# Kernel tuning notes

Measured on AMD Instinct MI355X. Metric: run time of the kernel, lower is better.

## Reference

```python
import jax, jax.numpy as jnp
import numpy as np

D_MODEL = 1024
N_HEADS = 16
D_HEAD = D_MODEL // N_HEADS
D_FF = 4096
THETA = 10000.0
EPS = 1e-5


def rmsnorm(x, g):
    xf = x.astype(jnp.float32)
    rms = jnp.sqrt(jnp.mean(xf * xf, axis=-1, keepdims=True) + EPS)
    return ((xf / rms) * g).astype(x.dtype)


def rope(x, pos):
    # x: (B, H, S, d_head); pos: (S,) int
    dk = x.shape[-1]
    inv_freq = 1.0 / (THETA ** (jnp.arange(0, dk, 2, dtype=jnp.float32) / dk))
    freqs = pos.astype(jnp.float32)[:, None] * inv_freq[None, :]  # (S, dk/2)
    cos, sin = jnp.cos(freqs), jnp.sin(freqs)
    xp = x.reshape(*x.shape[:-1], dk // 2, 2)
    xe, xo = xp[..., 0], xp[..., 1]
    re = xe * cos - xo * sin
    ro = xe * sin + xo * cos
    return jnp.stack([re, ro], axis=-1).reshape(x.shape)


def attention(x, pos, q_w, k_w, v_w, o_w):
    B, S, D = x.shape
    def heads(t):
        return t.reshape(B, S, N_HEADS, D_HEAD).transpose(0, 2, 1, 3)
    Q = heads(x @ q_w.T)
    K = heads(x @ k_w.T)
    V = heads(x @ v_w.T)
    Q = rope(Q, pos)
    K = rope(K, pos)
    scores = jnp.einsum('bhqd,bhkd->bhqk', Q, K) / jnp.sqrt(jnp.float32(D_HEAD))
    causal = jnp.tril(jnp.ones((S, S), dtype=bool))
    scores = jnp.where(causal[None, None], scores, -jnp.inf)
    attn = jax.nn.softmax(scores, axis=-1)
    H = jnp.einsum('bhqk,bhkd->bhqd', attn, V)
    H = H.transpose(0, 2, 1, 3).reshape(B, S, D)
    return H @ o_w.T


def swiglu(x, w1, w2, w3):
    a = x @ w1.T
    swish = a * jax.nn.sigmoid(a)
    gate = x @ w3.T
    return (swish * gate) @ w2.T


def setup_inputs() -> dict:
    key = jax.random.key(0)
    ks = jax.random.split(key, 8)
    B, S = 4, 2048
    std_ff = (2.0 / (D_MODEL + D_FF)) ** 0.5
    return {
        'x': jax.random.normal(ks[0], (B, S, D_MODEL), jnp.float32),
        'token_positions': jnp.arange(S, dtype=jnp.int32),
        'q_w': jax.random.truncated_normal(ks[1], -3, 3, (D_MODEL, D_MODEL), jnp.float32),
        'k_w': jax.random.truncated_normal(ks[2], -3, 3, (D_MODEL, D_MODEL), jnp.float32),
        'v_w': jax.random.truncated_normal(ks[3], -3, 3, (D_MODEL, D_MODEL), jnp.float32),
        'o_w': jax.random.truncated_normal(ks[4], -3, 3, (D_MODEL, D_MODEL), jnp.float32),
        'g1': jnp.ones((D_MODEL,), jnp.float32),
        'g2': jnp.ones((D_MODEL,), jnp.float32),
        'w1': jax.random.truncated_normal(ks[5], -3, 3, (D_FF, D_MODEL), jnp.float32) * std_ff,
        'w2': jax.random.truncated_normal(ks[6], -3, 3, (D_MODEL, D_FF), jnp.float32) * std_ff,
        'w3': jax.random.truncated_normal(ks[7], -3, 3, (D_FF, D_MODEL), jnp.float32) * std_ff,
    }


def reference(x, token_positions, q_w, k_w, v_w, o_w, g1, g2, w1, w2, w3):
    x_norm = rmsnorm(x, g1)
    O = x + attention(x_norm, token_positions, q_w, k_w, v_w, o_w)
    H = O + swiglu(rmsnorm(O, g2), w1, w2, w3)
    return H
```

## Files before the change

kernel.cpp:

```cpp
#include <hip/hip_runtime.h>
#include <stdint.h>


typedef short bf16x8 __attribute__((ext_vector_type(8)));
typedef float f32x4  __attribute__((ext_vector_type(4)));

#define DEV static __device__ __forceinline__

DEV float bf2f(uint32_t u) { uint32_t v = u << 16; float f; __builtin_memcpy(&f, &v, 4); return f; }
DEV uint16_t f2bf(float f) {
  uint32_t u; __builtin_memcpy(&u, &f, 4);
  u = (u + 0x7fffu + ((u >> 16) & 1u)) >> 16;
  return (uint16_t)u;
}

DEV void gl_lds16(const uint16_t* g, uint16_t* l) {
  __builtin_amdgcn_global_load_lds((const __attribute__((address_space(1))) uint32_t*)g,
                                   (__attribute__((address_space(3))) uint32_t*)l, 16, 0, 0);
}


__global__ __launch_bounds__(256) void cvt_bf16_k(const float* __restrict__ src,
                                                  uint16_t* __restrict__ dst, int n4) {
  const int t = blockIdx.x * 256 + threadIdx.x;
  if (t >= n4) return;
  const float4 v = ((const float4*)src)[t];
  ushort4 o; o.x = f2bf(v.x); o.y = f2bf(v.y); o.z = f2bf(v.z); o.w = f2bf(v.w);
  ((ushort4*)dst)[t] = o;
}

__global__ __launch_bounds__(256) void cvt_split_qk_k(const float* __restrict__ qw,
                                                      const float* __restrict__ kw,
                                                      uint16_t* __restrict__ hi,
                                                      uint16_t* __restrict__ lo) {
  const int t = blockIdx.x * 256 + threadIdx.x;
  const int row = t >> 8, c4 = t & 255;
  const float* src = (row < 1024) ? (qw + (size_t)row * 1024)
                                  : (kw + (size_t)(row - 1024) * 1024);
  const float4 v = ((const float4*)src)[c4];
  ushort4 h, l;
  h.x = f2bf(v.x); l.x = f2bf(v.x - bf2f(h.x));
  h.y = f2bf(v.y); l.y = f2bf(v.y - bf2f(h.y));
  h.z = f2bf(v.z); l.z = f2bf(v.z - bf2f(h.z));
  h.w = f2bf(v.w); l.w = f2bf(v.w - bf2f(h.w));
  ((ushort4*)hi)[t] = h; ((ushort4*)lo)[t] = l;
}


__global__ __launch_bounds__(256) void cs_tab_k(const int* __restrict__ pos,
                                                float2* __restrict__ tab) {
  const int t = blockIdx.x * 256 + threadIdx.x;
  const int p = t >> 5, d2 = t & 31;
  const float inv_freq = exp2f((float)d2 * -0.41524101186092029f);
  float sn, cs; sincosf((float)pos[p] * inv_freq, &sn, &cs);
  tab[t] = make_float2(cs, sn);
}


template <bool SPLIT>
__global__ __launch_bounds__(256) void rmsnorm_k(const float* __restrict__ xin,
                                                 const float* __restrict__ g,
                                                 uint16_t* __restrict__ hi,
                                                 uint16_t* __restrict__ lo) {
  const int row = blockIdx.x, t = threadIdx.x;
  const float4 v = ((const float4*)(xin + (size_t)row * 1024))[t];
  float ss = v.x * v.x + v.y * v.y + v.z * v.z + v.w * v.w;
#pragma unroll
  for (int m = 1; m < 64; m <<= 1) ss += __shfl_xor(ss, m);
  __shared__ float red[4];
  if ((t & 63) == 0) red[t >> 6] = ss;
  __syncthreads();
  const float rinv = rsqrtf((red[0] + red[1] + red[2] + red[3]) * (1.0f / 1024.0f) + 1e-5f);
  const float4 gv = ((const float4*)g)[t];
  float y[4] = { v.x * rinv * gv.x, v.y * rinv * gv.y, v.z * rinv * gv.z, v.w * rinv * gv.w };
  ushort4 h; h.x = f2bf(y[0]); h.y = f2bf(y[1]); h.z = f2bf(y[2]); h.w = f2bf(y[3]);
  ((ushort4*)(hi + (size_t)row * 1024))[t] = h;
  if constexpr (SPLIT) {
    ushort4 l;
    l.x = f2bf(y[0] - bf2f(h.x)); l.y = f2bf(y[1] - bf2f(h.y));
    l.z = f2bf(y[2] - bf2f(h.z)); l.w = f2bf(y[3] - bf2f(h.w));
    ((ushort4*)(lo + (size_t)row * 1024))[t] = l;
  }
}


template <int OUT>
__global__ __launch_bounds__(256) void gemm_bt_k(const uint16_t* __restrict__ A,
                                                 const uint16_t* __restrict__ B,
                                                 void* __restrict__ C,
                                                 const float* __restrict__ resid,
                                                 int N, int K) {
  __shared__ __align__(16) uint16_t As[128 * 64];
  __shared__ __align__(16) uint16_t Bs[128 * 64];
  const int t = threadIdx.x, w = t >> 6, lane = t & 63, m16 = lane & 15, quad = lane >> 4;
  const int wm = (w >> 1) * 64, wn = (w & 1) * 64;
  const int mBase = blockIdx.y * 128, nBase = blockIdx.x * 128;
  f32x4 acc[4][4];
  const f32x4 vz = {0.f, 0.f, 0.f, 0.f};
#pragma unroll
  for (int i = 0; i < 4; ++i)
#pragma unroll
    for (int j = 0; j < 4; ++j) acc[i][j] = vz;
  const int r_ = t >> 3, g_ = t & 7, sg = g_ ^ (r_ & 7);
  const uint16_t* ag = A + (size_t)(mBase + r_) * K + sg * 8;
  const uint16_t* bg = B + (size_t)(nBase + r_) * K + sg * 8;
  for (int k0 = 0; k0 < K; k0 += 64) {
#pragma unroll
    for (int it = 0; it < 4; ++it) {
      gl_lds16(ag + (size_t)(it * 32) * K + k0, As + it * 2048 + t * 8);
      gl_lds16(bg + (size_t)(it * 32) * K + k0, Bs + it * 2048 + t * 8);
    }
    __syncthreads();
#pragma unroll
    for (int ks = 0; ks < 2; ++ks) {
      bf16x8 af[4], bf4[4];
      const int cg = ks * 4 + quad;
#pragma unroll
      for (int i = 0; i < 4; ++i) {
        const int rA = wm + i * 16 + m16;
        af[i] = *(const bf16x8*)(As + rA * 64 + ((cg ^ (rA & 7)) * 8));
        const int rB = wn + i * 16 + m16;
        bf4[i] = *(const bf16x8*)(Bs + rB * 64 + ((cg ^ (rB & 7)) * 8));
      }
#pragma unroll
      for (int i = 0; i < 4; ++i)
#pragma unroll
        for (int j = 0; j < 4; ++j)
          acc[i][j] = __builtin_amdgcn_mfma_f32_16x16x32_bf16(af[i], bf4[j], acc[i][j], 0, 0, 0);
    }
    __syncthreads();
  }
#pragma unroll
  for (int i = 0; i < 4; ++i) {
    const int row0 = mBase + wm + i * 16 + quad * 4;
#pragma unroll
    for (int j = 0; j < 4; ++j) {
      const int col = nBase + wn + j * 16 + m16;
#pragma unroll
      for (int r = 0; r < 4; ++r) {
        const size_t idx = (size_t)(row0 + r) * N + col;
        const float v = acc[i][j][r];
        if constexpr (OUT == 1) ((float*)C)[idx] = v + resid[idx];
        else                    ((uint16_t*)C)[idx] = f2bf(v);
      }
    }
  }
}


template <int OUT>
__global__ __launch_bounds__(512, 2) void gemm256_k(const uint16_t* __restrict__ A,
                                                    const uint16_t* __restrict__ B,
                                                    uint16_t* __restrict__ C,
                                                    const uint16_t* __restrict__ aux,
                                                    int N, int K) {
  __shared__ __align__(16) uint16_t As[2][256 * 64];
  __shared__ __align__(16) uint16_t Bs[2][256 * 64];
  const int t = threadIdx.x, w = t >> 6, lane = t & 63, m16 = lane & 15, quad = lane >> 4;
  const int wm = (w >> 2) * 128, wn = (w & 3) * 64;
  const int mBase = blockIdx.y * 256, nBase = blockIdx.x * 256;
  const int NT = K >> 6;

  f32x4 acc[8][4];
  const f32x4 vz = {0.f, 0.f, 0.f, 0.f};
#pragma unroll
  for (int i = 0; i < 8; ++i)
#pragma unroll
    for (int j = 0; j < 4; ++j) acc[i][j] = vz;

  const int r_ = t >> 3, g_ = t & 7, sg = g_ ^ (r_ & 7);
  const uint16_t* ag = A + (size_t)(mBase + r_) * K + sg * 8;
  const uint16_t* bg = B + (size_t)(nBase + r_) * K + sg * 8;

#define STG_A(kt, h)                                                         \
  if ((kt) < NT) {                                                           \
    uint16_t* d0 = &As[(kt) & 1][(h) * 8192 + t * 8];                        \
    const uint16_t* s0 = ag + (size_t)((h) * 128) * K + (kt) * 64;           \
    gl_lds16(s0, d0);                                                        \
    gl_lds16(s0 + (size_t)64 * K, d0 + 4096);                                \
  }
#define STG_B(kt, h)                                                         \
  if ((kt) < NT) {                                                           \
    uint16_t* d0 = &Bs[(kt) & 1][(h) * 8192 + t * 8];                        \
    const uint16_t* s0 = bg + (size_t)((h) * 128) * K + (kt) * 64;           \
    gl_lds16(s0, d0);                                                        \
    gl_lds16(s0 + (size_t)64 * K, d0 + 4096);                                \
  }

  STG_B(0, 0); STG_B(0, 1); STG_A(0, 0); STG_A(0, 1);
  STG_B(1, 0); STG_A(1, 0);

  for (int T = 0; T < NT; ++T) {
    const int c = T & 1;
    const uint16_t* Ac = As[c];
    const uint16_t* Bc = Bs[c];
    bf16x8 af[4][2], b0[2][2], b1[2][2];

    STG_B(T + 1, 1);
    if (T == NT - 1) { asm volatile("s_waitcnt vmcnt(0)" ::: "memory"); }
    else             { asm volatile("s_waitcnt vmcnt(6)" ::: "memory"); }
    __builtin_amdgcn_s_barrier();
    __builtin_amdgcn_sched_barrier(0);
#pragma unroll
    for (int i = 0; i < 4; ++i) {
      const int rA = wm + i * 16 + m16;
#pragma unroll
      for (int ks = 0; ks < 2; ++ks)
        af[i][ks] = *(const bf16x8*)(Ac + rA * 64 + (((ks * 4 + quad) ^ (rA & 7)) * 8));
    }
#pragma unroll
    for (int j = 0; j < 2; ++j) {
      const int rB = wn + j * 16 + m16;
#pragma unroll
      for (int ks = 0; ks < 2; ++ks)
        b0[j][ks] = *(const bf16x8*)(Bc + rB * 64 + (((ks * 4 + quad) ^ (rB & 7)) * 8));
    }
    __builtin_amdgcn_s_setprio(1);
#pragma unroll
    for (int ks = 0; ks < 2; ++ks)
#pragma unroll
      for (int i = 0; i < 4; ++i)
#pragma unroll
        for (int j = 0; j < 2; ++j)
          acc[i][j] = __builtin_amdgcn_mfma_f32_16x16x32_bf16(af[i][ks], b0[j][ks], acc[i][j], 0, 0, 0);
    __builtin_amdgcn_s_setprio(0);
    __builtin_amdgcn_s_barrier();

    STG_A(T + 1, 1);
#pragma unroll
    for (int j = 0; j < 2; ++j) {
      const int rB = wn + (2 + j) * 16 + m16;
#pragma unroll
      for (int ks = 0; ks < 2; ++ks)
        b1[j][ks] = *(const bf16x8*)(Bc + rB * 64 + (((ks * 4 + quad) ^ (rB & 7)) * 8));
    }
    __builtin_amdgcn_s_setprio(1);
#pragma unroll
    for (int ks = 0; ks < 2; ++ks)
#pragma unroll
      for (int i = 0; i < 4; ++i)
#pragma unroll
        for (int j = 0; j < 2; ++j)
          acc[i][2 + j] = __builtin_amdgcn_mfma_f32_16x16x32_bf16(af[i][ks], b1[j][ks], acc[i][2 + j], 0, 0, 0);
    __builtin_amdgcn_s_setprio(0);
    __builtin_amdgcn_s_barrier();

    STG_B(T + 2, 0);
#pragma unroll
    for (int i = 0; i < 4; ++i) {
      const int rA = wm + 64 + i * 16 + m16;
#pragma unroll
      for (int ks = 0; ks < 2; ++ks)
        af[i][ks] = *(const bf16x8*)(Ac + rA * 64 + (((ks * 4 + quad) ^ (rA & 7)) * 8));
    }
    __builtin_amdgcn_s_setprio(1);
#pragma unroll
    for (int ks = 0; ks < 2; ++ks)
#pragma unroll
      for (int i = 0; i < 4; ++i)
#pragma unroll
        for (int j = 0; j < 2; ++j)
          acc[4 + i][j] = __builtin_amdgcn_mfma_f32_16x16x32_bf16(af[i][ks], b0[j][ks], acc[4 + i][j], 0, 0, 0);
    __builtin_amdgcn_s_setprio(0);
    __builtin_amdgcn_s_barrier();

    STG_A(T + 2, 0);
    __builtin_amdgcn_s_setprio(1);
#pragma unroll
    for (int ks = 0; ks < 2; ++ks)
#pragma unroll
      for (int i = 0; i < 4; ++i)
#pragma unroll
        for (int j = 0; j < 2; ++j)
          acc[4 + i][2 + j] = __builtin_amdgcn_mfma_f32_16x16x32_bf16(af[i][ks], b1[j][ks], acc[4 + i][2 + j], 0, 0, 0);
    __builtin_amdgcn_s_setprio(0);
    __builtin_amdgcn_s_barrier();
  }
#undef STG_A
#undef STG_B

#pragma unroll
  for (int i = 0; i < 8; ++i) {
    const int row0 = mBase + wm + i * 16 + quad * 4;
#pragma unroll
    for (int j = 0; j < 4; ++j) {
      const int col = nBase + wn + j * 16 + m16;
#pragma unroll
      for (int r = 0; r < 4; ++r) {
        const size_t idx = (size_t)(row0 + r) * N + col;
        const float v = acc[i][j][r];
        if constexpr (OUT == 2) {
          const float a = bf2f(aux[idx]);
          const float sw = a / (1.f + __expf(-a));
          C[idx] = f2bf(sw * v);
        } else {
          C[idx] = f2bf(v);
        }
      }
    }
  }
}


__global__ __launch_bounds__(512, 2) void gemm_split256_k(
    const uint16_t* __restrict__ Ahi, const uint16_t* __restrict__ Alo,
    const uint16_t* __restrict__ Bhi, const uint16_t* __restrict__ Blo,
    uint16_t* __restrict__ Chi, uint16_t* __restrict__ Clo,
    const float2* __restrict__ cstab, int N, int K) {
  __shared__ __align__(16) uint16_t Ah[2][256 * 32];
  __shared__ __align__(16) uint16_t Al[2][256 * 32];
  __shared__ __align__(16) uint16_t Bh[2][256 * 32];
  __shared__ __align__(16) uint16_t Bl[2][256 * 32];
  const int t = threadIdx.x, w = t >> 6, lane = t & 63, m16 = lane & 15, quad = lane >> 4;
  const int wm = (w >> 2) * 128, wn = (w & 3) * 64;
  const int mBase = blockIdx.y * 256, nBase = blockIdx.x * 256;
  const int NT = K >> 5;

  f32x4 acc[8][4];
  const f32x4 vz = {0.f, 0.f, 0.f, 0.f};
#pragma unroll
  for (int i = 0; i < 8; ++i)
#pragma unroll
    for (int j = 0; j < 4; ++j) acc[i][j] = vz;

  const int r_ = t >> 2, g_ = t & 3, sg = g_ ^ (r_ & 3);
  const uint16_t* agh = Ahi + (size_t)(mBase + r_) * K + sg * 8;
  const uint16_t* agl = Alo + (size_t)(mBase + r_) * K + sg * 8;
  const uint16_t* bgh = Bhi + (size_t)(nBase + r_) * K + sg * 8;
  const uint16_t* bgl = Blo + (size_t)(nBase + r_) * K + sg * 8;

#define STG4(OP, base, kt)                                                   \
  if ((kt) < NT) {                                                           \
    uint16_t* d = &OP[(kt) & 1][t * 8];                                      \
    const uint16_t* s = (base) + (size_t)(kt) * 32;                          \
    gl_lds16(s, d);                                                          \
    gl_lds16(s + (size_t)128 * K, d + 4096);                                 \
  }

  STG4(Bh, bgh, 0); STG4(Bl, bgl, 0);
  STG4(Ah, agh, 0); STG4(Al, agl, 0);
  STG4(Bh, bgh, 1); STG4(Bl, bgl, 1);

  for (int T = 0; T < NT; ++T) {
    const int c = T & 1;
    bf16x8 a_h[4], a_l[4], b0h[2], b0l[2], b1h[2], b1l[2];

    STG4(Ah, agh, T + 1);
    if (T == NT - 1) { asm volatile("s_waitcnt vmcnt(0)" ::: "memory"); }
    else             { asm volatile("s_waitcnt vmcnt(6)" ::: "memory"); }
    __builtin_amdgcn_s_barrier();
    __builtin_amdgcn_sched_barrier(0);
#pragma unroll
    for (int i = 0; i < 4; ++i) {
      const int rA = wm + i * 16 + m16;
      const int offA = rA * 32 + ((quad ^ (rA & 3)) * 8);
      a_h[i] = *(const bf16x8*)(&Ah[c][offA]);
      a_l[i] = *(const bf16x8*)(&Al[c][offA]);
    }
#pragma unroll
    for (int j = 0; j < 2; ++j) {
      const int rB = wn + j * 16 + m16;
      const int offB = rB * 32 + ((quad ^ (rB & 3)) * 8);
      b0h[j] = *(const bf16x8*)(&Bh[c][offB]);
      b0l[j] = *(const bf16x8*)(&Bl[c][offB]);
    }
    __builtin_amdgcn_s_setprio(1);
#pragma unroll
    for (int i = 0; i < 4; ++i)
#pragma unroll
      for (int j = 0; j < 2; ++j) {
        acc[i][j] = __builtin_amdgcn_mfma_f32_16x16x32_bf16(a_h[i], b0h[j], acc[i][j], 0, 0, 0);
        acc[i][j] = __builtin_amdgcn_mfma_f32_16x16x32_bf16(a_h[i], b0l[j], acc[i][j], 0, 0, 0);
        acc[i][j] = __builtin_amdgcn_mfma_f32_16x16x32_bf16(a_l[i], b0h[j], acc[i][j], 0, 0, 0);
      }
    __builtin_amdgcn_s_setprio(0);
    __builtin_amdgcn_s_barrier();

    STG4(Al, agl, T + 1);
#pragma unroll
    for (int j = 0; j < 2; ++j) {
      const int rB = wn + (2 + j) * 16 + m16;
      const int offB = rB * 32 + ((quad ^ (rB & 3)) * 8);
      b1h[j] = *(const bf16x8*)(&Bh[c][offB]);
      b1l[j] = *(const bf16x8*)(&Bl[c][offB]);
    }
    __builtin_amdgcn_s_setprio(1);
#pragma unroll
    for (int i = 0; i < 4; ++i)
#pragma unroll
      for (int j = 0; j < 2; ++j) {
        acc[i][2 + j] = __builtin_amdgcn_mfma_f32_16x16x32_bf16(a_h[i], b1h[j], acc[i][2 + j], 0, 0, 0);
        acc[i][2 + j] = __builtin_amdgcn_mfma_f32_16x16x32_bf16(a_h[i], b1l[j], acc[i][2 + j], 0, 0, 0);
        acc[i][2 + j] = __builtin_amdgcn_mfma_f32_16x16x32_bf16(a_l[i], b1h[j], acc[i][2 + j], 0, 0, 0);
      }
    __builtin_amdgcn_s_setprio(0);
    __builtin_amdgcn_s_barrier();

    STG4(Bh, bgh, T + 2);
#pragma unroll
    for (int i = 0; i < 4; ++i) {
      const int rA = wm + 64 + i * 16 + m16;
      const int offA = rA * 32 + ((quad ^ (rA & 3)) * 8);
      a_h[i] = *(const bf16x8*)(&Ah[c][offA]);
      a_l[i] = *(const bf16x8*)(&Al[c][offA]);
    }
    __builtin_amdgcn_s_setprio(1);
#pragma unroll
    for (int i = 0; i < 4; ++i)
#pragma unroll
      for (int j = 0; j < 2; ++j) {
        acc[4 + i][j] = __builtin_amdgcn_mfma_f32_16x16x32_bf16(a_h[i], b0h[j], acc[4 + i][j], 0, 0, 0);
        acc[4 + i][j] = __builtin_amdgcn_mfma_f32_16x16x32_bf16(a_h[i], b0l[j], acc[4 + i][j], 0, 0, 0);
        acc[4 + i][j] = __builtin_amdgcn_mfma_f32_16x16x32_bf16(a_l[i], b0h[j], acc[4 + i][j], 0, 0, 0);
      }
    __builtin_amdgcn_s_setprio(0);
    __builtin_amdgcn_s_barrier();

    STG4(Bl, bgl, T + 2);
    __builtin_amdgcn_s_setprio(1);
#pragma unroll
    for (int i = 0; i < 4; ++i)
#pragma unroll
      for (int j = 0; j < 2; ++j) {
        acc[4 + i][2 + j] = __builtin_amdgcn_mfma_f32_16x16x32_bf16(a_h[i], b1h[j], acc[4 + i][2 + j], 0, 0, 0);
        acc[4 + i][2 + j] = __builtin_amdgcn_mfma_f32_16x16x32_bf16(a_h[i], b1l[j], acc[4 + i][2 + j], 0, 0, 0);
        acc[4 + i][2 + j] = __builtin_amdgcn_mfma_f32_16x16x32_bf16(a_l[i], b1h[j], acc[4 + i][2 + j], 0, 0, 0);
      }
    __builtin_amdgcn_s_setprio(0);
    __builtin_amdgcn_s_barrier();
  }
#undef STG4

  int d2v[4];
#pragma unroll
  for (int j = 0; j < 4; ++j)
    d2v[j] = ((nBase + wn + j * 16 + m16) & 63) >> 1;
  const bool oddc = (m16 & 1) != 0;
#pragma unroll
  for (int i = 0; i < 8; ++i) {
    const int row0 = mBase + wm + i * 16 + quad * 4;
#pragma unroll
    for (int r = 0; r < 4; ++r) {
      const int row = row0 + r;
      const float2* crow = cstab + (size_t)(row & 2047) * 32;
      const size_t rb = (size_t)row * N;
#pragma unroll
      for (int j = 0; j < 4; ++j) {
        const float v = acc[i][j][r];
        const float pv = __shfl_xor(v, 1);
        const float xe = oddc ? pv : v;
        const float xo = oddc ? v : pv;
        const float2 cs = crow[d2v[j]];
        const float vr = oddc ? (xe * cs.y + xo * cs.x) : (xe * cs.x - xo * cs.y);
        const size_t idx = rb + (nBase + wn + j * 16 + m16);
        const uint16_t hh = f2bf(vr);
        Chi[idx] = hh;
        Clo[idx] = f2bf(vr - bf2f(hh));
      }
    }
  }
}


__global__ __launch_bounds__(256) void flash_k(const uint16_t* __restrict__ Qh,
                                               const uint16_t* __restrict__ Ql,
                                               const uint16_t* __restrict__ Vt,
                                               uint16_t* __restrict__ Hout) {
  __shared__ __align__(16) uint16_t Kh[2][64 * 64];
  __shared__ __align__(16) uint16_t Kl[2][64 * 64];
  __shared__ __align__(16) uint16_t Vs[2][64 * 64];
  __shared__ __align__(16) uint16_t P[4][32 * 72];

  const int bh = blockIdx.y, b = bh >> 4, h = bh & 15;
  const int t = threadIdx.x, w = t >> 6, lane = t & 63, m16 = lane & 15, quad = lane >> 4;

  const int r_ = t >> 3, g_ = t & 7, sgx = g_ ^ (r_ & 7);
  const uint16_t* khg = Qh + (size_t)(b * 2048 + r_) * 2048 + 1024 + h * 64 + sgx * 8;
  const uint16_t* klg = Ql + (size_t)(b * 2048 + r_) * 2048 + 1024 + h * 64 + sgx * 8;
  const uint16_t* vtg = Vt + (size_t)(h * 64 + r_) * 8192 + (size_t)b * 2048 + sgx * 8;

  const float nscl = 0.18033688011112042f;
  bf16x8 onef;
#pragma unroll
  for (int e = 0; e < 8; ++e) onef[e] = (short)0x3F80;

  for (int half = 0; half < 2; ++half) {
    const int qt = half ? (15 - (int)blockIdx.x) : (int)blockIdx.x;

    bf16x8 qh[2][2], ql[2][2];
#pragma unroll
    for (int i = 0; i < 2; ++i) {
      const int row = b * 2048 + qt * 128 + w * 32 + i * 16 + m16;
#pragma unroll
      for (int ks = 0; ks < 2; ++ks) {
        const size_t offq = (size_t)row * 2048 + h * 64 + ks * 32 + quad * 8;
        qh[i][ks] = *(const bf16x8*)(Qh + offq);
        ql[i][ks] = *(const bf16x8*)(Ql + offq);
      }
    }
#pragma unroll
    for (int i = 0; i < 2; ++i)
#pragma unroll
      for (int ks = 0; ks < 2; ++ks)
        asm volatile("" : "+v"(qh[i][ks]), "+v"(ql[i][ks]));

    const int ktEnd = 2 * qt + 2;

#pragma unroll
    for (int it = 0; it < 2; ++it) {
      gl_lds16(khg + (size_t)(it * 32) * 2048, &Kh[0][it * 2048 + t * 8]);
      gl_lds16(klg + (size_t)(it * 32) * 2048, &Kl[0][it * 2048 + t * 8]);
      gl_lds16(vtg + (size_t)(it * 32) * 8192, &Vs[0][it * 2048 + t * 8]);
    }

    float mr[2][4];
    f32x4 o[2][4], ls2[2];
    const f32x4 vz = {0.f, 0.f, 0.f, 0.f};
#pragma unroll
    for (int i = 0; i < 2; ++i)
#pragma unroll
      for (int r = 0; r < 4; ++r) mr[i][r] = -1e30f;
    ls2[0] = vz; ls2[1] = vz;
#pragma unroll
    for (int i = 0; i < 2; ++i)
#pragma unroll
      for (int n = 0; n < 4; ++n) o[i][n] = vz;

    for (int kt = 0; kt < ktEnd; ++kt) {
      const int cur = kt & 1, nxt = cur ^ 1;
      __builtin_amdgcn_s_barrier();
      __builtin_amdgcn_sched_barrier(0);
      if (kt + 1 < ktEnd) {
        const int kn = kt + 1;
#pragma unroll
        for (int it = 0; it < 2; ++it) {
          gl_lds16(khg + (size_t)(kn * 64 + it * 32) * 2048, &Kh[nxt][it * 2048 + t * 8]);
          gl_lds16(klg + (size_t)(kn * 64 + it * 32) * 2048, &Kl[nxt][it * 2048 + t * 8]);
          gl_lds16(vtg + (size_t)(it * 32) * 8192 + kn * 64, &Vs[nxt][it * 2048 + t * 8]);
        }
        asm volatile("s_waitcnt vmcnt(6)" ::: "memory");
      } else {
        asm volatile("s_waitcnt vmcnt(0)" ::: "memory");
      }
      __builtin_amdgcn_s_barrier();
      __builtin_amdgcn_sched_barrier(0);

      f32x4 sc[2][4];
#pragma unroll
      for (int i = 0; i < 2; ++i)
#pragma unroll
        for (int j = 0; j < 4; ++j) sc[i][j] = vz;
#pragma unroll
      for (int ks = 0; ks < 2; ++ks) {
        bf16x8 kfh[4], kfl[4];
        const int cg = ks * 4 + quad;
#pragma unroll
        for (int j = 0; j < 4; ++j) {
          const int rK = j * 16 + m16;
          const int offk = rK * 64 + ((cg ^ (rK & 7)) * 8);
          kfh[j] = *(const bf16x8*)(&Kh[cur][offk]);
          kfl[j] = *(const bf16x8*)(&Kl[cur][offk]);
        }
        __builtin_amdgcn_s_setprio(1);
#pragma unroll
        for (int i = 0; i < 2; ++i)
#pragma unroll
          for (int j = 0; j < 4; ++j) {
            sc[i][j] = __builtin_amdgcn_mfma_f32_16x16x32_bf16(qh[i][ks], kfh[j], sc[i][j], 0, 0, 0);
            sc[i][j] = __builtin_amdgcn_mfma_f32_16x16x32_bf16(qh[i][ks], kfl[j], sc[i][j], 0, 0, 0);
            sc[i][j] = __builtin_amdgcn_mfma_f32_16x16x32_bf16(ql[i][ks], kfh[j], sc[i][j], 0, 0, 0);
          }
        __builtin_amdgcn_s_setprio(0);
      }

#pragma unroll
      for (int i = 0; i < 2; ++i) {
        const bool needMask = (kt * 64 + 63) > (qt * 128 + w * 32 + i * 16);
#pragma unroll
        for (int r = 0; r < 4; ++r) {
          float mx = -1e30f;
          if (needMask) {
            const int qg = qt * 128 + w * 32 + i * 16 + quad * 4 + r;
#pragma unroll
            for (int j = 0; j < 4; ++j) {
              float v = sc[i][j][r];
              const int kg = kt * 64 + j * 16 + m16;
              if (kg > qg) v = -1e30f;
              sc[i][j][r] = v;
              mx = fmaxf(mx, v);
            }
          } else {
#pragma unroll
            for (int j = 0; j < 4; ++j) mx = fmaxf(mx, sc[i][j][r]);
          }
#pragma unroll
          for (int m = 1; m < 16; m <<= 1) mx = fmaxf(mx, __shfl_xor(mx, m));
          const float mnew = fmaxf(mr[i][r], mx);
          const float alpha = __builtin_amdgcn_exp2f((mr[i][r] - mnew) * nscl);
          mr[i][r] = mnew;
          const float nm = mnew * nscl;
#pragma unroll
          for (int j = 0; j < 4; ++j)
            sc[i][j][r] = __builtin_amdgcn_exp2f(__builtin_fmaf(sc[i][j][r], nscl, -nm));
          ls2[i][r] *= alpha;
#pragma unroll
          for (int n = 0; n < 4; ++n) o[i][n][r] *= alpha;
        }
#pragma unroll
        for (int j = 0; j < 4; ++j) {
          uint32_t pk01, pk23;
          asm("v_cvt_pk_bf16_f32 %0, %1, %2"
              : "=v"(pk01) : "v"(sc[i][j][0]), "v"(sc[i][j][1]));
          asm("v_cvt_pk_bf16_f32 %0, %1, %2"
              : "=v"(pk23) : "v"(sc[i][j][2]), "v"(sc[i][j][3]));
          const int pb = (i * 16 + quad * 4) * 72 + j * 16 + m16;
          P[w][pb]       = (uint16_t)pk01;
          P[w][pb + 72]  = (uint16_t)(pk01 >> 16);
          P[w][pb + 144] = (uint16_t)pk23;
          P[w][pb + 216] = (uint16_t)(pk23 >> 16);
        }
      }

#pragma unroll
      for (int ks2 = 0; ks2 < 2; ++ks2) {
        bf16x8 pf[2], vf[4];
#pragma unroll
        for (int i = 0; i < 2; ++i)
          pf[i] = *(const bf16x8*)(&P[w][(i * 16 + m16) * 72 + ks2 * 32 + quad * 8]);
        const int cg = ks2 * 4 + quad;
#pragma unroll
        for (int n = 0; n < 4; ++n) {
          const int rV = n * 16 + m16;
          vf[n] = *(const bf16x8*)(&Vs[cur][rV * 64 + ((cg ^ (rV & 7)) * 8)]);
        }
        __builtin_amdgcn_s_setprio(1);
#pragma unroll
        for (int i = 0; i < 2; ++i) {
          ls2[i] = __builtin_amdgcn_mfma_f32_16x16x32_bf16(pf[i], onef, ls2[i], 0, 0, 0);
#pragma unroll
          for (int n = 0; n < 4; ++n)
            o[i][n] = __builtin_amdgcn_mfma_f32_16x16x32_bf16(pf[i], vf[n], o[i][n], 0, 0, 0);
        }
        __builtin_amdgcn_s_setprio(0);
      }
    }

#pragma unroll
    for (int i = 0; i < 2; ++i)
#pragma unroll
      for (int r = 0; r < 4; ++r) {
        const float inv = 1.f / ls2[i][r];
        const size_t row = (size_t)(b * 2048 + qt * 128 + w * 32 + i * 16 + quad * 4 + r);
#pragma unroll
        for (int n = 0; n < 4; ++n)
          Hout[row * 1024 + h * 64 + n * 16 + m16] = f2bf(o[i][n][r] * inv);
      }
    __syncthreads();
  }
}


extern "C" void kernel_launch(void* const* d_in, const int* in_sizes, int n_in,
                              void* d_out, int out_size, void* d_ws, size_t ws_size,
                              hipStream_t stream) {
  (void)in_sizes; (void)n_in; (void)out_size; (void)ws_size;
  const float* x   = (const float*)d_in[0];
  const int*   pos = (const int*)  d_in[1];
  const float* q_w = (const float*)d_in[2];
  const float* k_w = (const float*)d_in[3];
  const float* v_w = (const float*)d_in[4];
  const float* o_w = (const float*)d_in[5];
  const float* g1  = (const float*)d_in[6];
  const float* g2  = (const float*)d_in[7];
  const float* w1  = (const float*)d_in[8];
  const float* w2  = (const float*)d_in[9];
  const float* w3  = (const float*)d_in[10];

  char* ws = (char*)d_ws;
  uint16_t* wqk_hi = (uint16_t*)(ws + 0);
  uint16_t* wqk_lo = (uint16_t*)(ws + 4194304);
  uint16_t* wv     = (uint16_t*)(ws + 8388608);
  uint16_t* wo     = (uint16_t*)(ws + 10485760);
  uint16_t* w1b    = (uint16_t*)(ws + 12582912);
  uint16_t* w3b    = (uint16_t*)(ws + 20971520);
  uint16_t* w2b    = (uint16_t*)(ws + 29360128);
  uint16_t* xn_hi  = (uint16_t*)(ws + 37748736);
  uint16_t* xn_lo  = (uint16_t*)(ws + 54525952);
  uint16_t* vt     = (uint16_t*)(ws + 88080384);
  uint16_t* qk_hi  = (uint16_t*)(ws + 104857600);
  uint16_t* qk_lo  = (uint16_t*)(ws + 138412032);
  uint16_t* hbuf   = (uint16_t*)(ws + 171966464);
  float*    ores   = (float*)   (ws + 188743680);
  uint16_t* on2    = (uint16_t*)(ws + 222298112);
  uint16_t* abuf   = (uint16_t*)(ws + 104857600);
  uint16_t* gbuf   = (uint16_t*)(ws + 37748736);
  float2*   cstab  = (float2*)  (ws + 222298112);

  cvt_split_qk_k<<<2048, 256, 0, stream>>>(q_w, k_w, wqk_hi, wqk_lo);
  cvt_bf16_k<<<1024, 256, 0, stream>>>(v_w, wv, 262144);
  cvt_bf16_k<<<1024, 256, 0, stream>>>(o_w, wo, 262144);
  cvt_bf16_k<<<4096, 256, 0, stream>>>(w1, w1b, 1048576);
  cvt_bf16_k<<<4096, 256, 0, stream>>>(w3, w3b, 1048576);
  cvt_bf16_k<<<4096, 256, 0, stream>>>(w2, w2b, 1048576);
  cs_tab_k<<<256, 256, 0, stream>>>(pos, cstab);

  rmsnorm_k<true><<<8192, 256, 0, stream>>>(x, g1, xn_hi, xn_lo);

  gemm_split256_k<<<dim3(8, 32), 512, 0, stream>>>(xn_hi, xn_lo, wqk_hi, wqk_lo,
                                                   qk_hi, qk_lo, cstab, 2048, 1024);
  gemm_bt_k<0><<<dim3(64, 8), 256, 0, stream>>>(wv, xn_hi, (void*)vt, nullptr, 8192, 1024);

  flash_k<<<dim3(8, 64), 256, 0, stream>>>(qk_hi, qk_lo, vt, hbuf);

  gemm_bt_k<1><<<dim3(8, 64), 256, 0, stream>>>(hbuf, wo, (void*)ores, x, 1024, 1024);

  rmsnorm_k<false><<<8192, 256, 0, stream>>>(ores, g2, on2, nullptr);

  gemm256_k<0><<<dim3(16, 32), 512, 0, stream>>>(on2, w1b, abuf, nullptr, 4096, 1024);
  gemm256_k<2><<<dim3(16, 32), 512, 0, stream>>>(on2, w3b, gbuf, abuf, 4096, 1024);

  gemm_bt_k<1><<<dim3(8, 64), 256, 0, stream>>>(gbuf, w2b, d_out, ores, 1024, 4096);
}
```

Baseline: 766.7 us.

## Fuse weight conversions into one launch and single-buffer K tiles in flash attention

The five fp32-to-bf16 weight conversion launches and the RoPE cos/sin table launch are merged into one kernel that picks its source by block index, cutting launch overhead. In the flash attention kernel, the K hi/lo tiles go from double-buffered to single-buffered LDS. The next K tile is loaded only after a new barrier placed after the QK MFMAs, while V stays double-buffered. This lowers LDS use, which may allow more blocks per CU, but adds a barrier per tile and exposes K load latency behind the softmax and PV work only.

```diff
diff --git a/kernel.cpp b/kernel.cpp
--- a/kernel.cpp
+++ b/kernel.cpp
@@ -20,10 +20,28 @@
 }
 
 
-__global__ __launch_bounds__(256) void cvt_bf16_k(const float* __restrict__ src,
-                                                  uint16_t* __restrict__ dst, int n4) {
-  const int t = blockIdx.x * 256 + threadIdx.x;
-  if (t >= n4) return;
+__global__ __launch_bounds__(256) void cvt_all_k(
+    const float* __restrict__ v_w, const float* __restrict__ o_w,
+    const float* __restrict__ w1, const float* __restrict__ w3,
+    const float* __restrict__ w2, const int* __restrict__ pos,
+    uint16_t* __restrict__ wv, uint16_t* __restrict__ wo,
+    uint16_t* __restrict__ w1b, uint16_t* __restrict__ w3b,
+    uint16_t* __restrict__ w2b, float2* __restrict__ cstab) {
+  const int b = blockIdx.x;
+  if (b >= 14336) {
+    const int t = (b - 14336) * 256 + threadIdx.x;
+    const int p = t >> 5, d2 = t & 31;
+    const float inv_freq = exp2f((float)d2 * -0.41524101186092029f);
+    float sn, cs; sincosf((float)pos[p] * inv_freq, &sn, &cs);
+    cstab[t] = make_float2(cs, sn);
+    return;
+  }
+  const float* src; uint16_t* dst; int t;
+  if (b < 1024)       { src = v_w; dst = wv;  t = b * 256 + threadIdx.x; }
+  else if (b < 2048)  { src = o_w; dst = wo;  t = (b - 1024) * 256 + threadIdx.x; }
+  else if (b < 6144)  { src = w1;  dst = w1b; t = (b - 2048) * 256 + threadIdx.x; }
+  else if (b < 10240) { src = w3;  dst = w3b; t = (b - 6144) * 256 + threadIdx.x; }
+  else                { src = w2;  dst = w2b; t = (b - 10240) * 256 + threadIdx.x; }
   const float4 v = ((const float4*)src)[t];
   ushort4 o; o.x = f2bf(v.x); o.y = f2bf(v.y); o.z = f2bf(v.z); o.w = f2bf(v.w);
   ((ushort4*)dst)[t] = o;
@@ -47,16 +65,6 @@
 }
 
 
-__global__ __launch_bounds__(256) void cs_tab_k(const int* __restrict__ pos,
-                                                float2* __restrict__ tab) {
-  const int t = blockIdx.x * 256 + threadIdx.x;
-  const int p = t >> 5, d2 = t & 31;
-  const float inv_freq = exp2f((float)d2 * -0.41524101186092029f);
-  float sn, cs; sincosf((float)pos[p] * inv_freq, &sn, &cs);
-  tab[t] = make_float2(cs, sn);
-}
-
-
 template <bool SPLIT>
 __global__ __launch_bounds__(256) void rmsnorm_k(const float* __restrict__ xin,
                                                  const float* __restrict__ g,
@@ -466,8 +474,8 @@
                                                const uint16_t* __restrict__ Ql,
                                                const uint16_t* __restrict__ Vt,
                                                uint16_t* __restrict__ Hout) {
-  __shared__ __align__(16) uint16_t Kh[2][64 * 64];
-  __shared__ __align__(16) uint16_t Kl[2][64 * 64];
+  __shared__ __align__(16) uint16_t Kh[64 * 64];
+  __shared__ __align__(16) uint16_t Kl[64 * 64];
   __shared__ __align__(16) uint16_t Vs[2][64 * 64];
   __shared__ __align__(16) uint16_t P[4][32 * 72];
 
@@ -508,10 +516,12 @@
 
 #pragma unroll
     for (int it = 0; it < 2; ++it) {
-      gl_lds16(khg + (size_t)(it * 32) * 2048, &Kh[0][it * 2048 + t * 8]);
-      gl_lds16(klg + (size_t)(it * 32) * 2048, &Kl[0][it * 2048 + t * 8]);
+      gl_lds16(khg + (size_t)(it * 32) * 2048, &Kh[it * 2048 + t * 8]);
+      gl_lds16(klg + (size_t)(it * 32) * 2048, &Kl[it * 2048 + t * 8]);
+    }
+#pragma unroll
+    for (int it = 0; it < 2; ++it)
       gl_lds16(vtg + (size_t)(it * 32) * 8192, &Vs[0][it * 2048 + t * 8]);
-    }
 
     float mr[2][4];
     f32x4 o[2][4], ls2[2];
@@ -531,14 +541,11 @@
       __builtin_amdgcn_s_barrier();
       __builtin_amdgcn_sched_barrier(0);
       if (kt + 1 < ktEnd) {
-        const int kn = kt + 1;
-#pragma unroll
-        for (int it = 0; it < 2; ++it) {
-          gl_lds16(khg + (size_t)(kn * 64 + it * 32) * 2048, &Kh[nxt][it * 2048 + t * 8]);
-          gl_lds16(klg + (size_t)(kn * 64 + it * 32) * 2048, &Kl[nxt][it * 2048 + t * 8]);
-          gl_lds16(vtg + (size_t)(it * 32) * 8192 + kn * 64, &Vs[nxt][it * 2048 + t * 8]);
-        }
-        asm volatile("s_waitcnt vmcnt(6)" ::: "memory");
+#pragma unroll
+        for (int it = 0; it < 2; ++it)
+          gl_lds16(vtg + (size_t)(it * 32) * 8192 + (kt + 1) * 64,
+                   &Vs[nxt][it * 2048 + t * 8]);
+        asm volatile("s_waitcnt vmcnt(2)" ::: "memory");
       } else {
         asm volatile("s_waitcnt vmcnt(0)" ::: "memory");
       }
@@ -558,8 +565,8 @@
         for (int j = 0; j < 4; ++j) {
           const int rK = j * 16 + m16;
           const int offk = rK * 64 + ((cg ^ (rK & 7)) * 8);
-          kfh[j] = *(const bf16x8*)(&Kh[cur][offk]);
-          kfl[j] = *(const bf16x8*)(&Kl[cur][offk]);
+          kfh[j] = *(const bf16x8*)(&Kh[offk]);
+          kfl[j] = *(const bf16x8*)(&Kl[offk]);
         }
         __builtin_amdgcn_s_setprio(1);
 #pragma unroll
@@ -571,6 +578,16 @@
             sc[i][j] = __builtin_amdgcn_mfma_f32_16x16x32_bf16(ql[i][ks], kfh[j], sc[i][j], 0, 0, 0);
           }
         __builtin_amdgcn_s_setprio(0);
+      }
+
+      __builtin_amdgcn_s_barrier();
+      __builtin_amdgcn_sched_barrier(0);
+      if (kt + 1 < ktEnd) {
+#pragma unroll
+        for (int it = 0; it < 2; ++it) {
+          gl_lds16(khg + (size_t)((kt + 1) * 64 + it * 32) * 2048, &Kh[it * 2048 + t * 8]);
+          gl_lds16(klg + (size_t)((kt + 1) * 64 + it * 32) * 2048, &Kl[it * 2048 + t * 8]);
+        }
       }
 
 #pragma unroll
@@ -697,12 +714,8 @@
   float2*   cstab  = (float2*)  (ws + 222298112);
 
   cvt_split_qk_k<<<2048, 256, 0, stream>>>(q_w, k_w, wqk_hi, wqk_lo);
-  cvt_bf16_k<<<1024, 256, 0, stream>>>(v_w, wv, 262144);
-  cvt_bf16_k<<<1024, 256, 0, stream>>>(o_w, wo, 262144);
-  cvt_bf16_k<<<4096, 256, 0, stream>>>(w1, w1b, 1048576);
-  cvt_bf16_k<<<4096, 256, 0, stream>>>(w3, w3b, 1048576);
-  cvt_bf16_k<<<4096, 256, 0, stream>>>(w2, w2b, 1048576);
-  cs_tab_k<<<256, 256, 0, stream>>>(pos, cstab);
+  cvt_all_k<<<14592, 256, 0, stream>>>(v_w, o_w, w1, w3, w2, pos,
+                                       wv, wo, w1b, w3b, w2b, cstab);
 
   rmsnorm_k<true><<<8192, 256, 0, stream>>>(x, g1, xn_hi, xn_lo);
 
```

After: 767.8 us. Within noise of the previous version (+0.1%).
